# Performance work log

Hardware: AMD Instinct MI355X
Metric: run time of the kernel (lower is better)

Reference implementation:

```python
import jax, jax.numpy as jnp
import numpy as np

D_MODEL = 1024
NUM_HEADS = 16
D_K = D_MODEL // NUM_HEADS
B, S = 2, 2048


def setup_inputs() -> dict:
    key = jax.random.key(0)
    ks = jax.random.split(key, 9)
    scale = 1.0 / np.sqrt(D_MODEL)
    return {
        "hidden_states": jax.random.normal(ks[0], (B, S, D_MODEL), dtype=jnp.float32),
        "attention_mask": jnp.ones((B, S, S), dtype=jnp.int32),
        "Wq": jax.random.normal(ks[1], (D_MODEL, D_MODEL), dtype=jnp.float32) * scale,
        "bq": jnp.zeros((D_MODEL,), dtype=jnp.float32),
        "Wk": jax.random.normal(ks[2], (D_MODEL, D_MODEL), dtype=jnp.float32) * scale,
        "bk": jnp.zeros((D_MODEL,), dtype=jnp.float32),
        "Wv": jax.random.normal(ks[3], (D_MODEL, D_MODEL), dtype=jnp.float32) * scale,
        "bv": jnp.zeros((D_MODEL,), dtype=jnp.float32),
        "Wo": jax.random.normal(ks[4], (D_MODEL, D_MODEL), dtype=jnp.float32) * scale,
        "bo": jnp.zeros((D_MODEL,), dtype=jnp.float32),
    }


def reference(hidden_states, attention_mask, Wq, bq, Wk, bk, Wv, bv, Wo, bo):
    b, s, _ = hidden_states.shape
    # torch Linear: y = x @ W.T + b
    def proj(W, bias):
        y = jnp.einsum('bsd,ed->bse', hidden_states, W) + bias
        return y.reshape(b, s, NUM_HEADS, D_K).transpose(0, 2, 1, 3)  # [B,H,S,dk]
    q = proj(Wq, bq)
    k = proj(Wk, bk)
    v = proj(Wv, bv)
    scores = jnp.einsum('bnqd,bnkd->bnqk', q, k) / np.sqrt(D_K)
    mask = attention_mask[:, None, :, :]  # [B,1,S,S]
    scores = jnp.where(mask == 0, jnp.float32(-1e9), scores)
    attn = jax.nn.softmax(scores, axis=-1)  # dropout = identity (eval)
    ctx = jnp.einsum('bnqk,bnkd->bnqd', attn, v)
    ctx = ctx.transpose(0, 2, 1, 3).reshape(b, s, D_MODEL)
    return jnp.einsum('bsd,ed->bse', ctx, Wo) + bo
```

## Files before the change

### kernel.cpp

```cpp
#include <hip/hip_runtime.h>

typedef short short8 __attribute__((ext_vector_type(8)));
typedef float floatx4 __attribute__((ext_vector_type(4)));
typedef float floatx16 __attribute__((ext_vector_type(16)));
typedef unsigned short ushort4v __attribute__((ext_vector_type(4)));

#define DEV static __device__ __forceinline__

DEV unsigned short f2bf(float f) {
  unsigned int u = __builtin_bit_cast(unsigned int, f);
  u += 0x7fffu + ((u >> 16) & 1u);
  return (unsigned short)(u >> 16);
}

DEV unsigned int cvtpk(float a, float b) {
  unsigned int r;
  asm("v_cvt_pk_bf16_f32 %0, %1, %2" : "=v"(r) : "v"(a), "v"(b));
  return r;
}

DEV void gload16(const unsigned short* g, unsigned short* l) {
  __builtin_amdgcn_global_load_lds((__attribute__((address_space(1))) void*)g,
                                   (__attribute__((address_space(3))) void*)l,
                                   16, 0, 0);
}

__global__ void convert_kernel(const float* __restrict__ hs, const float* __restrict__ Wq,
                               const float* __restrict__ Wk, const float* __restrict__ Wv,
                               const float* __restrict__ Wo,
                               unsigned short* __restrict__ xbf, unsigned short* __restrict__ wqkv,
                               unsigned short* __restrict__ wobf) {
  size_t i4 = ((size_t)blockIdx.x * 256 + threadIdx.x) * 4;
  const float* src;
  unsigned short* dst;
  if (i4 < 4194304) {
    src = hs + i4; dst = xbf + i4;
  } else if (i4 < 7340032) {
    size_t o = i4 - 4194304;
    size_t lo = o & 1048575;
    src = (o < 1048576) ? (Wq + lo) : ((o < 2097152) ? (Wk + lo) : (Wv + lo));
    dst = wqkv + o;
  } else {
    size_t o = i4 - 7340032;
    src = Wo + o; dst = wobf + o;
  }
  float4 v = *(const float4*)src;
  ushort4v u;
  u.x = f2bf(v.x); u.y = f2bf(v.y); u.z = f2bf(v.z); u.w = f2bf(v.w);
  *(ushort4v*)dst = u;
}

__global__ void maskpack_kernel(const int* __restrict__ mask, unsigned long long* __restrict__ bits) {
  int w = blockIdx.x * 256 + threadIdx.x;
  const int4* p = (const int4*)(mask + (size_t)w * 64);
  unsigned long long r = 0ull;
#pragma unroll
  for (int j = 0; j < 16; ++j) {
    int4 m = p[j];
    r |= (unsigned long long)(m.x != 0) << (j * 4 + 0);
    r |= (unsigned long long)(m.y != 0) << (j * 4 + 1);
    r |= (unsigned long long)(m.z != 0) << (j * 4 + 2);
    r |= (unsigned long long)(m.w != 0) << (j * 4 + 3);
  }
  bits[w] = r;
}

__global__ void __launch_bounds__(256) qkv_gemm(
    const unsigned short* __restrict__ X, const unsigned short* __restrict__ W,
    const float* __restrict__ bq, const float* __restrict__ bk, const float* __restrict__ bv,
    unsigned short* __restrict__ Qb, unsigned short* __restrict__ Kb,
    unsigned short* __restrict__ Vt) {
  __shared__ __align__(16) unsigned short As[128 * 32];
  __shared__ __align__(16) unsigned short Bs[128 * 32];
  const int tid = threadIdx.x;
  const int lane = tid & 63, wv = tid >> 6;
  const int wm = wv >> 1, wn = wv & 1;
  const int quad = lane >> 4, l15 = lane & 15;
  const int mb = blockIdx.y, nb = blockIdx.x;
  const bool sw = (nb < 16);

  const unsigned short* ga = X + (size_t)(mb * 128 + (tid >> 2)) * 1024 + (tid & 3) * 8;
  const unsigned short* gb = W + (size_t)(nb * 128 + (tid >> 2)) * 1024 + (tid & 3) * 8;
  unsigned short* la1 = As + tid * 8;
  unsigned short* la2 = As + 2048 + tid * 8;
  unsigned short* lb1 = Bs + tid * 8;
  unsigned short* lb2 = Bs + 2048 + tid * 8;

  const int wx = sw ? wn : wm;
  const int ww = sw ? wm : wn;

  floatx4 acc[4][4] = {};
  for (int kt = 0; kt < 32; ++kt) {
    const int k0 = kt * 32;
    gload16(ga + k0, la1);
    gload16(ga + k0 + 65536, la2);
    gload16(gb + k0, lb1);
    gload16(gb + k0 + 65536, lb2);
    __syncthreads();
    short8 xa[4], wb[4];
#pragma unroll
    for (int i = 0; i < 4; ++i) {
      xa[i] = *(const short8*)&As[(wx * 64 + i * 16 + l15) * 32 + quad * 8];
      wb[i] = *(const short8*)&Bs[(ww * 64 + i * 16 + l15) * 32 + quad * 8];
    }
    if (sw) {
#pragma unroll
      for (int mt = 0; mt < 4; ++mt)
#pragma unroll
        for (int nt = 0; nt < 4; ++nt)
          acc[mt][nt] = __builtin_amdgcn_mfma_f32_16x16x32_bf16(wb[mt], xa[nt], acc[mt][nt], 0, 0, 0);
    } else {
#pragma unroll
      for (int mt = 0; mt < 4; ++mt)
#pragma unroll
        for (int nt = 0; nt < 4; ++nt)
          acc[mt][nt] = __builtin_amdgcn_mfma_f32_16x16x32_bf16(xa[mt], wb[nt], acc[mt][nt], 0, 0, 0);
    }
    __syncthreads();
  }

  if (sw) {
#pragma unroll
    for (int mt = 0; mt < 4; ++mt) {
      const int wc0 = nb * 128 + wm * 64 + mt * 16 + quad * 4;
      const int mat = wc0 >> 10;
      const int nl0 = wc0 & 1023;
      const int hh = nl0 >> 6, d0 = nl0 & 63;
      const float4 b4 = *(const float4*)((mat ? bk : bq) + nl0);
      unsigned short* dst = mat ? Kb : Qb;
#pragma unroll
      for (int nt = 0; nt < 4; ++nt) {
        const int colx = mb * 128 + wn * 64 + nt * 16 + l15;
        const int bb = colx >> 11, s = colx & 2047;
        ushort4v pv;
        pv[0] = f2bf(acc[mt][nt][0] + b4.x);
        pv[1] = f2bf(acc[mt][nt][1] + b4.y);
        pv[2] = f2bf(acc[mt][nt][2] + b4.z);
        pv[3] = f2bf(acc[mt][nt][3] + b4.w);
        *(ushort4v*)&dst[((size_t)(bb * 16 + hh) * 2048 + s) * 64 + d0] = pv;
      }
    }
  } else {
#pragma unroll
    for (int nt = 0; nt < 4; ++nt) {
      const int col = nb * 128 + wn * 64 + nt * 16 + l15;
      const int nl = col & 1023;
      const float bias = bv[nl];
      const int hh = nl >> 6, d = nl & 63;
#pragma unroll
      for (int mt = 0; mt < 4; ++mt) {
        const int row0 = mb * 128 + wm * 64 + mt * 16 + quad * 4;
        const int bb = row0 >> 11, s = row0 & 2047;
        ushort4v pv;
#pragma unroll
        for (int r = 0; r < 4; ++r) pv[r] = f2bf(acc[mt][nt][r] + bias);
        *(ushort4v*)&Vt[((size_t)(bb * 16 + hh) * 64 + d) * 2048 + s] = pv;
      }
    }
  }
}

__global__ void __launch_bounds__(256, 2) attn_kernel(
    const unsigned short* __restrict__ Qb, const unsigned short* __restrict__ Kb,
    const unsigned short* __restrict__ Vt, const unsigned long long* __restrict__ mbits,
    unsigned short* __restrict__ ctx) {
  __shared__ __align__(16) unsigned short SM[4 * 64 * 64];
  const int tid = threadIdx.x;
  const int lane = tid & 63, wv = tid >> 6;
  const int l31 = lane & 31, h = lane >> 5;
  const int qg = wv & 1, h2 = wv >> 1;
  const int bid = (blockIdx.x & 7) * 128 + (blockIdx.x >> 3);
  const int pair = bid >> 5, qt = bid & 31;
  const int b_ = pair >> 4, hd = pair & 15;
  const int qrow = qt * 64 + qg * 32 + l31;
  const size_t pbase = (size_t)pair * (2048 * 64);
  const size_t vtb = (size_t)pair * (64 * 2048);

  short8 qf[4];
#pragma unroll
  for (int ks = 0; ks < 4; ++ks)
    qf[ks] = *(const short8*)(Qb + pbase + (size_t)qrow * 64 + ks * 16 + h * 8);

  unsigned short* Kh = SM + h2 * 4096;
  unsigned short* Vh = SM + 8192 + h2 * 4096;

  const int kLane = (lane >> 3) * 64 + (((lane & 7) ^ (lane >> 3)) * 8);
  const int vLane = (lane >> 3) * 2048 + (((lane & 7) ^ (lane >> 3)) * 8);
  const int cb = qg * 4;

  const unsigned long long* mrow = mbits + ((size_t)b_ * 2048 + qrow) * 32;

  floatx16 acc_o[2] = {};
  float lacc[2] = {0.f, 0.f};
  const float SCL = 0.125f * 1.44269504088896340736f;
  const float NC = -10.0f;

  for (int it = 0; it < 16; ++it) {
    const int tg = h2 * 16 + it;
    const unsigned short* kt = Kb + pbase + (size_t)tg * 4096;
    const unsigned short* vt = Vt + vtb + (size_t)tg * 64;
#pragma unroll
    for (int i = 0; i < 4; ++i) {
      gload16(kt + (cb + i) * 512 + kLane, Kh + (cb + i) * 512 + lane * 8);
      gload16(vt + (size_t)(cb + i) * 16384 + vLane, Vh + (cb + i) * 512 + lane * 8);
    }
    const unsigned long long w = mrow[tg];
    __syncthreads();

    floatx16 accs[2] = {};
    __builtin_amdgcn_s_setprio(1);
#pragma unroll
    for (int ks = 0; ks < 4; ++ks)
#pragma unroll
      for (int kb = 0; kb < 2; ++kb) {
        const int krow = kb * 32 + l31;
        short8 kf = *(const short8*)&Kh[krow * 64 + (((ks * 2 + h) ^ (krow & 7)) * 8)];
        accs[kb] = __builtin_amdgcn_mfma_f32_32x32x16_bf16(kf, qf[ks], accs[kb], 0, 0, 0);
      }
    __builtin_amdgcn_s_setprio(0);

    if (__any(w != ~0ull)) {
#pragma unroll
      for (int kb = 0; kb < 2; ++kb)
#pragma unroll
        for (int reg = 0; reg < 16; ++reg) {
          const int kl = (reg & 3) + 8 * (reg >> 2) + 4 * h;
          const int bit = kb * 32 + kl;
          if (!((w >> bit) & 1ull)) accs[kb][reg] = -6e9f;
        }
    }

#pragma unroll
    for (int kb = 0; kb < 2; ++kb) {
      unsigned int pk[8];
      float ls = 0.f;
#pragma unroll
      for (int i = 0; i < 8; ++i) {
        const float a = exp2f(fmaf(accs[kb][2 * i], SCL, NC));
        const float b = exp2f(fmaf(accs[kb][2 * i + 1], SCL, NC));
        ls += a + b;
        pk[i] = cvtpk(a, b);
      }
      lacc[kb] += ls;
#pragma unroll
      for (int u = 0; u < 2; ++u) {
        auto r02 = __builtin_amdgcn_permlane32_swap(pk[4 * u + 0], pk[4 * u + 2], false, false);
        auto r13 = __builtin_amdgcn_permlane32_swap(pk[4 * u + 1], pk[4 * u + 3], false, false);
        union { unsigned int wd[4]; short8 s8; } af;
        af.wd[0] = r02[0];
        af.wd[1] = r13[0];
        af.wd[2] = r02[1];
        af.wd[3] = r13[1];
        const int t = kb * 2 + u;
        __builtin_amdgcn_s_setprio(1);
#pragma unroll
        for (int nt = 0; nt < 2; ++nt) {
          const int vrow = nt * 32 + l31;
          short8 vf = *(const short8*)&Vh[vrow * 64 + (((t * 2 + h) ^ (vrow & 7)) * 8)];
          acc_o[nt] = __builtin_amdgcn_mfma_f32_32x32x16_bf16(af.s8, vf, acc_o[nt], 0, 0, 0);
        }
        __builtin_amdgcn_s_setprio(0);
      }
    }
    __syncthreads();
  }

  float lsum = lacc[0] + lacc[1];
  lsum += __shfl_xor(lsum, 32);

  float* red = (float*)SM;
  if (h2 == 1) {
    float* p = red + (qg * 64 + lane) * 33;
#pragma unroll
    for (int reg = 0; reg < 16; ++reg) {
      p[reg] = acc_o[0][reg];
      p[16 + reg] = acc_o[1][reg];
    }
    p[32] = lsum;
  }
  __syncthreads();
  if (h2 == 0) {
    const float* p = red + (qg * 64 + lane) * 33;
#pragma unroll
    for (int reg = 0; reg < 16; ++reg) {
      acc_o[0][reg] += p[reg];
      acc_o[1][reg] += p[16 + reg];
    }
    lsum += p[32];
    const float rinv = 1.f / ((lsum > 0.f) ? lsum : 1.f);
#pragma unroll
    for (int reg = 0; reg < 16; ++reg) {
      const int ql = (reg & 3) + 8 * (reg >> 2) + 4 * h;
      const float rl = __shfl(rinv, ql);
      const size_t base = ((size_t)b_ * 2048 + qt * 64 + qg * 32 + ql) * 1024 + hd * 64;
      ctx[base + l31]      = f2bf(acc_o[0][reg] * rl);
      ctx[base + 32 + l31] = f2bf(acc_o[1][reg] * rl);
    }
  }
}

__global__ void __launch_bounds__(256) out_gemm(
    const unsigned short* __restrict__ C, const unsigned short* __restrict__ W,
    const float* __restrict__ bo, float* __restrict__ out) {
  __shared__ __align__(16) unsigned short As[128 * 32];
  __shared__ __align__(16) unsigned short Bs[128 * 32];
  const int tid = threadIdx.x;
  const int lane = tid & 63, wv = tid >> 6;
  const int wm = wv >> 1, wn = wv & 1;
  const int quad = lane >> 4, l15 = lane & 15;
  const int mb = blockIdx.y, nb = blockIdx.x;

  const unsigned short* ga = C + (size_t)(mb * 128 + (tid >> 2)) * 1024 + (tid & 3) * 8;
  const unsigned short* gb = W + (size_t)(nb * 128 + (tid >> 2)) * 1024 + (tid & 3) * 8;
  unsigned short* la1 = As + tid * 8;
  unsigned short* la2 = As + 2048 + tid * 8;
  unsigned short* lb1 = Bs + tid * 8;
  unsigned short* lb2 = Bs + 2048 + tid * 8;

  floatx4 acc[4][4] = {};
  for (int kt = 0; kt < 32; ++kt) {
    const int k0 = kt * 32;
    gload16(ga + k0, la1);
    gload16(ga + k0 + 65536, la2);
    gload16(gb + k0, lb1);
    gload16(gb + k0 + 65536, lb2);
    __syncthreads();
    short8 af[4], bfr[4];
#pragma unroll
    for (int i = 0; i < 4; ++i) {
      af[i]  = *(const short8*)&As[(wm * 64 + i * 16 + l15) * 32 + quad * 8];
      bfr[i] = *(const short8*)&Bs[(wn * 64 + i * 16 + l15) * 32 + quad * 8];
    }
#pragma unroll
    for (int mt = 0; mt < 4; ++mt)
#pragma unroll
      for (int nt = 0; nt < 4; ++nt)
        acc[mt][nt] = __builtin_amdgcn_mfma_f32_16x16x32_bf16(af[mt], bfr[nt], acc[mt][nt], 0, 0, 0);
    __syncthreads();
  }
#pragma unroll
  for (int nt = 0; nt < 4; ++nt) {
    const int col = nb * 128 + wn * 64 + nt * 16 + l15;
    const float bias = bo[col];
#pragma unroll
    for (int mt = 0; mt < 4; ++mt)
#pragma unroll
      for (int r = 0; r < 4; ++r) {
        const int row = mb * 128 + wm * 64 + mt * 16 + quad * 4 + r;
        out[(size_t)row * 1024 + col] = acc[mt][nt][r] + bias;
      }
  }
}

extern "C" void kernel_launch(void* const* d_in, const int* in_sizes, int n_in,
                              void* d_out, int out_size, void* d_ws, size_t ws_size,
                              hipStream_t stream) {
  const float* hs = (const float*)d_in[0];
  const int* mask = (const int*)d_in[1];
  const float* Wq = (const float*)d_in[2];
  const float* bq = (const float*)d_in[3];
  const float* Wk = (const float*)d_in[4];
  const float* bk = (const float*)d_in[5];
  const float* Wv = (const float*)d_in[6];
  const float* bv = (const float*)d_in[7];
  const float* Wo = (const float*)d_in[8];
  const float* bo = (const float*)d_in[9];
  float* out = (float*)d_out;

  char* ws = (char*)d_ws;
  unsigned short* xbf  = (unsigned short*)(ws + 0);
  unsigned short* wqkv = (unsigned short*)(ws + 8388608);
  unsigned short* wobf = (unsigned short*)(ws + 14680064);
  unsigned short* Qb   = (unsigned short*)(ws + 16777216);
  unsigned short* Kb   = (unsigned short*)(ws + 25165824);
  unsigned short* Vt   = (unsigned short*)(ws + 33554432);
  unsigned short* ctx  = (unsigned short*)(ws + 41943040);
  unsigned long long* mbits = (unsigned long long*)(ws + 50331648);

  convert_kernel<<<8192, 256, 0, stream>>>(hs, Wq, Wk, Wv, Wo, xbf, wqkv, wobf);
  maskpack_kernel<<<512, 256, 0, stream>>>(mask, mbits);
  qkv_gemm<<<dim3(24, 32), 256, 0, stream>>>(xbf, wqkv, bq, bk, bv, Qb, Kb, Vt);
  attn_kernel<<<1024, 256, 0, stream>>>(Qb, Kb, Vt, mbits, ctx);
  out_gemm<<<dim3(8, 32), 256, 0, stream>>>(ctx, wobf, bo, out);
}
```

Baseline: 256.8 us.

## Double-buffer K/V tiles with 32-key steps and prefetch next tile

Restructures the attention inner loop to process 32-key tiles over 32 iterations and double-buffer the shared-memory K and V tiles. The loads for the next tile are issued before the current tile's compute, so only one barrier per iteration remains and global-load latency can overlap with the MFMA work. K and V loading is now split between wave groups (one loads K, the other V), and the V tile gets a new 32-wide swizzle. The cost is more loop iterations with less compute per barrier, and the same 32KB of shared memory is now used as two smaller buffers.

```diff
diff --git a/kernel.cpp b/kernel.cpp
--- a/kernel.cpp
+++ b/kernel.cpp
@@ -164,7 +164,7 @@
     const unsigned short* __restrict__ Qb, const unsigned short* __restrict__ Kb,
     const unsigned short* __restrict__ Vt, const unsigned long long* __restrict__ mbits,
     unsigned short* __restrict__ ctx) {
-  __shared__ __align__(16) unsigned short SM[4 * 64 * 64];
+  __shared__ __align__(16) unsigned short SM[16384];
   const int tid = threadIdx.x;
   const int lane = tid & 63, wv = tid >> 6;
   const int l31 = lane & 31, h = lane >> 5;
@@ -181,91 +181,100 @@
   for (int ks = 0; ks < 4; ++ks)
     qf[ks] = *(const short8*)(Qb + pbase + (size_t)qrow * 64 + ks * 16 + h * 8);
 
-  unsigned short* Kh = SM + h2 * 4096;
-  unsigned short* Vh = SM + 8192 + h2 * 4096;
-
-  const int kLane = (lane >> 3) * 64 + (((lane & 7) ^ (lane >> 3)) * 8);
-  const int vLane = (lane >> 3) * 2048 + (((lane & 7) ^ (lane >> 3)) * 8);
-  const int cb = qg * 4;
-
-  const unsigned long long* mrow = mbits + ((size_t)b_ * 2048 + qrow) * 32;
+  const int kSrc = (lane >> 3) * 64 + (((lane & 7) ^ (lane >> 3)) * 8);
+  const int vSrc = (lane >> 2) * 2048 + (((lane & 3) ^ ((lane >> 3) & 3)) * 8);
+
+  const unsigned short* kgb = Kb + pbase + (size_t)h2 * (1024 * 64);
+  const unsigned short* vgb = Vt + vtb + h2 * 1024;
+  unsigned short* ldK = SM + h2 * 4096 + lane * 8;
+  unsigned short* ldV = SM + h2 * 4096 + 2048 + lane * 8;
+
+  const unsigned long long* mrow = mbits + ((size_t)b_ * 2048 + qrow) * 32 + h2 * 16;
 
   floatx16 acc_o[2] = {};
-  float lacc[2] = {0.f, 0.f};
+  float lsum = 0.f;
   const float SCL = 0.125f * 1.44269504088896340736f;
   const float NC = -10.0f;
 
-  for (int it = 0; it < 16; ++it) {
-    const int tg = h2 * 16 + it;
-    const unsigned short* kt = Kb + pbase + (size_t)tg * 4096;
-    const unsigned short* vt = Vt + vtb + (size_t)tg * 64;
-#pragma unroll
-    for (int i = 0; i < 4; ++i) {
-      gload16(kt + (cb + i) * 512 + kLane, Kh + (cb + i) * 512 + lane * 8);
-      gload16(vt + (size_t)(cb + i) * 16384 + vLane, Vh + (cb + i) * 512 + lane * 8);
-    }
-    const unsigned long long w = mrow[tg];
-    __syncthreads();
-
-    floatx16 accs[2] = {};
+  if (qg == 0) {
+#pragma unroll
+    for (int i = 0; i < 4; ++i) gload16(kgb + kSrc + i * 512, ldK + i * 512);
+  } else {
+#pragma unroll
+    for (int i = 0; i < 4; ++i) gload16(vgb + vSrc + (size_t)i * 32768, ldV + i * 512);
+  }
+  __syncthreads();
+
+  for (int it = 0; it < 32; ++it) {
+    const int cur = it & 1;
+    const unsigned short* Kh = SM + cur * 8192 + h2 * 4096;
+    const unsigned short* Vh = Kh + 2048;
+
+    if (it < 31) {
+      const int nb = cur ^ 1;
+      if (qg == 0) {
+        const unsigned short* s = kgb + (size_t)(it + 1) * 2048 + kSrc;
+        unsigned short* d = ldK + nb * 8192;
+#pragma unroll
+        for (int i = 0; i < 4; ++i) gload16(s + i * 512, d + i * 512);
+      } else {
+        const unsigned short* s = vgb + (size_t)(it + 1) * 32 + vSrc;
+        unsigned short* d = ldV + nb * 8192;
+#pragma unroll
+        for (int i = 0; i < 4; ++i) gload16(s + (size_t)i * 32768, d + i * 512);
+      }
+    }
+    const unsigned long long w = mrow[it >> 1];
+    const int bitbase = (it & 1) * 32;
+
+    floatx16 accs = {};
     __builtin_amdgcn_s_setprio(1);
 #pragma unroll
-    for (int ks = 0; ks < 4; ++ks)
-#pragma unroll
-      for (int kb = 0; kb < 2; ++kb) {
-        const int krow = kb * 32 + l31;
-        short8 kf = *(const short8*)&Kh[krow * 64 + (((ks * 2 + h) ^ (krow & 7)) * 8)];
-        accs[kb] = __builtin_amdgcn_mfma_f32_32x32x16_bf16(kf, qf[ks], accs[kb], 0, 0, 0);
-      }
+    for (int ks = 0; ks < 4; ++ks) {
+      short8 kf = *(const short8*)&Kh[l31 * 64 + (((ks * 2 + h) ^ (l31 & 7)) * 8)];
+      accs = __builtin_amdgcn_mfma_f32_32x32x16_bf16(kf, qf[ks], accs, 0, 0, 0);
+    }
     __builtin_amdgcn_s_setprio(0);
 
     if (__any(w != ~0ull)) {
 #pragma unroll
-      for (int kb = 0; kb < 2; ++kb)
-#pragma unroll
-        for (int reg = 0; reg < 16; ++reg) {
-          const int kl = (reg & 3) + 8 * (reg >> 2) + 4 * h;
-          const int bit = kb * 32 + kl;
-          if (!((w >> bit) & 1ull)) accs[kb][reg] = -6e9f;
-        }
-    }
-
-#pragma unroll
-    for (int kb = 0; kb < 2; ++kb) {
-      unsigned int pk[8];
-      float ls = 0.f;
-#pragma unroll
-      for (int i = 0; i < 8; ++i) {
-        const float a = exp2f(fmaf(accs[kb][2 * i], SCL, NC));
-        const float b = exp2f(fmaf(accs[kb][2 * i + 1], SCL, NC));
-        ls += a + b;
-        pk[i] = cvtpk(a, b);
-      }
-      lacc[kb] += ls;
-#pragma unroll
-      for (int u = 0; u < 2; ++u) {
-        auto r02 = __builtin_amdgcn_permlane32_swap(pk[4 * u + 0], pk[4 * u + 2], false, false);
-        auto r13 = __builtin_amdgcn_permlane32_swap(pk[4 * u + 1], pk[4 * u + 3], false, false);
-        union { unsigned int wd[4]; short8 s8; } af;
-        af.wd[0] = r02[0];
-        af.wd[1] = r13[0];
-        af.wd[2] = r02[1];
-        af.wd[3] = r13[1];
-        const int t = kb * 2 + u;
-        __builtin_amdgcn_s_setprio(1);
-#pragma unroll
-        for (int nt = 0; nt < 2; ++nt) {
-          const int vrow = nt * 32 + l31;
-          short8 vf = *(const short8*)&Vh[vrow * 64 + (((t * 2 + h) ^ (vrow & 7)) * 8)];
-          acc_o[nt] = __builtin_amdgcn_mfma_f32_32x32x16_bf16(af.s8, vf, acc_o[nt], 0, 0, 0);
-        }
-        __builtin_amdgcn_s_setprio(0);
-      }
-    }
-    __syncthreads();
-  }
-
-  float lsum = lacc[0] + lacc[1];
+      for (int reg = 0; reg < 16; ++reg) {
+        const int kl = (reg & 3) + 8 * (reg >> 2) + 4 * h;
+        if (!((w >> (bitbase + kl)) & 1ull)) accs[reg] = -6e9f;
+      }
+    }
+
+    unsigned int pk[8];
+    float ls = 0.f;
+#pragma unroll
+    for (int i = 0; i < 8; ++i) {
+      const float a = exp2f(fmaf(accs[2 * i], SCL, NC));
+      const float b = exp2f(fmaf(accs[2 * i + 1], SCL, NC));
+      ls += a + b;
+      pk[i] = cvtpk(a, b);
+    }
+    lsum += ls;
+#pragma unroll
+    for (int u = 0; u < 2; ++u) {
+      auto r02 = __builtin_amdgcn_permlane32_swap(pk[4 * u + 0], pk[4 * u + 2], false, false);
+      auto r13 = __builtin_amdgcn_permlane32_swap(pk[4 * u + 1], pk[4 * u + 3], false, false);
+      union { unsigned int wd[4]; short8 s8; } af;
+      af.wd[0] = r02[0];
+      af.wd[1] = r13[0];
+      af.wd[2] = r02[1];
+      af.wd[3] = r13[1];
+      __builtin_amdgcn_s_setprio(1);
+#pragma unroll
+      for (int nt = 0; nt < 2; ++nt) {
+        const int vrow = nt * 32 + l31;
+        short8 vf = *(const short8*)&Vh[vrow * 32 + (((u * 2 + h) ^ ((vrow >> 1) & 3)) * 8)];
+        acc_o[nt] = __builtin_amdgcn_mfma_f32_32x32x16_bf16(af.s8, vf, acc_o[nt], 0, 0, 0);
+      }
+      __builtin_amdgcn_s_setprio(0);
+    }
+    __syncthreads();
+  }
+
   lsum += __shfl_xor(lsum, 32);
 
   float* red = (float*)SM;
```

After: 254.9 us. No clear change (-0.8%).
